# Kernel tuning notes

Hardware: AMD Instinct MI355X
Metric: run time of the kernel (lower is better)

Reference implementation:

```python
import jax, jax.numpy as jnp
import numpy as np

EPS = 1e-12  # matches F.normalize default eps

def _angle(e):
    # e: [N, D] embeddings
    d = e[:, None, :] - e[None, :, :]                      # [N, N, D] pairwise differences
    n = jnp.linalg.norm(d, axis=-1, keepdims=True)         # [N, N, 1]
    d = d / jnp.maximum(n, EPS)                            # normalized diffs; diagonal stays 0
    # all-triplet cosines: for each anchor i, Gram matrix of its normalized diffs
    return jnp.einsum('ijd,ikd->ijk', d, d)                # [N, N, N]

def _smooth_l1_mean(a, b):
    # torch F.smooth_l1_loss with beta=1.0, reduction='mean'
    x = jnp.abs(a - b)
    return jnp.mean(jnp.where(x < 1.0, 0.5 * x * x, x - 0.5))

def setup_inputs() -> dict:
    key = jax.random.key(0)
    k1, k2 = jax.random.split(key)
    student = jax.random.normal(k1, (384, 256), dtype=jnp.float32)
    teacher = jax.random.normal(k2, (384, 256), dtype=jnp.float32)
    return {"student": student, "teacher": teacher}

def reference(student, teacher):
    s_angle = _angle(student)
    t_angle = _angle(teacher)
    return _smooth_l1_mean(s_angle, t_angle)
```

## Files before the change

kernel.cpp:

```cpp
#include <hip/hip_runtime.h>
#include <hip/hip_bf16.h>

#define NPTS 384
#define NN (NPTS * NPTS)
#define DIMS 256
#define IT 8
#define NZI (NPTS / IT)

__global__ __launch_bounds__(1024) void gram_fused_kernel(
        const float* __restrict__ Es, const float* __restrict__ Et,
        float* __restrict__ Gs, float* __restrict__ Gt,
        float2* __restrict__ UHs, float2* __restrict__ UHt,
        float* __restrict__ out) {
    const int z = blockIdx.z;
    const float* __restrict__ E  = z ? Et : Es;
    float*       __restrict__ G  = z ? Gt : Gs;
    float2*      __restrict__ UH = z ? UHt : UHs;

    const int tx = threadIdx.x;
    const int ty = threadIdx.y;
    const int kc = threadIdx.z;
    const int t  = kc * 256 + ty * 16 + tx;
    const int i0 = blockIdx.x * 32;
    const int j0 = blockIdx.y * 32;

    if (blockIdx.x == 0 && blockIdx.y == 0 && z == 0 && t == 0) out[0] = 0.0f;

    __shared__ float sn[64];
    __shared__ float red[4][1024];

    {
        const int r = t >> 4;
        const int p = t & 15;
        const int row = (r < 32) ? (i0 + r) : (j0 + r - 32);
        const float4* __restrict__ src = (const float4*)(E + row * DIMS) + p * 4;
        float s = 0.f;
#pragma unroll
        for (int q = 0; q < 4; q++) {
            const float4 v = src[q];
            s += v.x * v.x + v.y * v.y + v.z * v.z + v.w * v.w;
        }
        s += __shfl_xor(s, 1, 64);
        s += __shfl_xor(s, 2, 64);
        s += __shfl_xor(s, 4, 64);
        s += __shfl_xor(s, 8, 64);
        if (p == 0) sn[r] = s;
    }

    const int i = i0 + 2 * ty;
    const int j = j0 + 2 * tx;
    const float4* __restrict__ a0 = (const float4*)(E + i * DIMS + kc * 64);
    const float4* __restrict__ a1 = (const float4*)(E + (i + 1) * DIMS + kc * 64);
    const float4* __restrict__ b0 = (const float4*)(E + j * DIMS + kc * 64);
    const float4* __restrict__ b1 = (const float4*)(E + (j + 1) * DIMS + kc * 64);

    float g00 = 0.f, g01 = 0.f, g10 = 0.f, g11 = 0.f;
#pragma unroll 4
    for (int k = 0; k < 16; k++) {
        const float4 av0 = a0[k], av1 = a1[k], bv0 = b0[k], bv1 = b1[k];
        g00 = fmaf(av0.x, bv0.x, g00); g00 = fmaf(av0.y, bv0.y, g00);
        g00 = fmaf(av0.z, bv0.z, g00); g00 = fmaf(av0.w, bv0.w, g00);
        g01 = fmaf(av0.x, bv1.x, g01); g01 = fmaf(av0.y, bv1.y, g01);
        g01 = fmaf(av0.z, bv1.z, g01); g01 = fmaf(av0.w, bv1.w, g01);
        g10 = fmaf(av1.x, bv0.x, g10); g10 = fmaf(av1.y, bv0.y, g10);
        g10 = fmaf(av1.z, bv0.z, g10); g10 = fmaf(av1.w, bv0.w, g10);
        g11 = fmaf(av1.x, bv1.x, g11); g11 = fmaf(av1.y, bv1.y, g11);
        g11 = fmaf(av1.z, bv1.z, g11); g11 = fmaf(av1.w, bv1.w, g11);
    }

    const int t2 = ty * 16 + tx;
    *(float4*)&red[kc][t2 * 4] = make_float4(g00, g01, g10, g11);
    __syncthreads();

    if (kc == 0) {
        const float4 r0 = *(const float4*)&red[0][t2 * 4];
        const float4 r1 = *(const float4*)&red[1][t2 * 4];
        const float4 r2 = *(const float4*)&red[2][t2 * 4];
        const float4 r3 = *(const float4*)&red[3][t2 * 4];
        const float g[2][2] = {{r0.x + r1.x + r2.x + r3.x, r0.y + r1.y + r2.y + r3.y},
                               {r0.z + r1.z + r2.z + r3.z, r0.w + r1.w + r2.w + r3.w}};
        const float si[2] = {sn[2 * ty], sn[2 * ty + 1]};
        const float sj[2] = {sn[32 + 2 * tx], sn[32 + 2 * tx + 1]};

#pragma unroll
        for (int r = 0; r < 2; r++) {
            const int ii = i + r;
            float uh[4];
#pragma unroll
            for (int c = 0; c < 2; c++) {
                const int jj = j + c;
                const float gv = g[r][c];
                const float v  = si[r] + sj[c] - 2.0f * gv;
                const float n  = sqrtf(fmaxf(v, 0.0f));
                uh[2 * c]     = (ii == jj) ? 0.0f : (1.0f / fmaxf(n, 1e-12f));
                uh[2 * c + 1] = 0.5f * si[r] - gv;
            }
            *(float2*)(G + ii * NPTS + j) = make_float2(g[r][0], g[r][1]);
            *(float4*)(UH + ii * NPTS + j) = make_float4(uh[0], uh[1], uh[2], uh[3]);
        }
    }
}

__global__ __launch_bounds__(256, 3) void rkd_main_kernel(
        const float* __restrict__ Gs, const float* __restrict__ Gt,
        const float2* __restrict__ UHs, const float2* __restrict__ UHt,
        float* __restrict__ out) {
    const int tlin = blockIdx.x;
    const int kt = (int)((sqrtf(8.0f * (float)tlin + 1.0f) - 1.0f) * 0.5f);
    const int jt = tlin - (kt * (kt + 1)) / 2;

    const int tx = threadIdx.x;
    const int ty = threadIdx.y;
    const int jb = jt * 64 + 4 * ty;
    const int kb = kt * 64 + 4 * tx;
    const int ibase = blockIdx.y * IT;

    float gs[4][4], gt[4][4];
#pragma unroll
    for (int a = 0; a < 4; a++) {
        const float4 vs = *(const float4*)(Gs + (jb + a) * NPTS + kb);
        const float4 vt = *(const float4*)(Gt + (jb + a) * NPTS + kb);
        gs[a][0] = vs.x; gs[a][1] = vs.y; gs[a][2] = vs.z; gs[a][3] = vs.w;
        gt[a][0] = vt.x; gt[a][1] = vt.y; gt[a][2] = vt.z; gt[a][3] = vt.w;
    }

    const float4* __restrict__ pjs = (const float4*)(UHs + (size_t)ibase * NPTS + jb);
    const float4* __restrict__ pjt = (const float4*)(UHt + (size_t)ibase * NPTS + jb);
    const float4* __restrict__ pks = (const float4*)(UHs + (size_t)ibase * NPTS + kb);
    const float4* __restrict__ pkt = (const float4*)(UHt + (size_t)ibase * NPTS + kb);

    const bool offd = (jt != kt);
    float wh[4][4];
#pragma unroll
    for (int a = 0; a < 4; a++)
#pragma unroll
        for (int b = 0; b < 4; b++) {
            const int jj = jb + a, kk = kb + b;
            wh[a][b] = (kk > jj) ? 1.0f : ((kk == jj) ? 0.5f : 0.0f);
        }

    float4 L[8];
    L[0] = pjs[0]; L[1] = pjs[1];
    L[2] = pjt[0]; L[3] = pjt[1];
    L[4] = pks[0]; L[5] = pks[1];
    L[6] = pkt[0]; L[7] = pkt[1];

    float acc = 0.0f;
#pragma unroll 2
    for (int iz = 0; iz < IT; iz++) {
        const int nz = (iz + 1 < IT) ? iz + 1 : iz;
        const int ro = nz * (NPTS / 2);
        float4 Ln[8];
        Ln[0] = pjs[ro];     Ln[1] = pjs[ro + 1];
        Ln[2] = pjt[ro];     Ln[3] = pjt[ro + 1];
        Ln[4] = pks[ro];     Ln[5] = pks[ro + 1];
        Ln[6] = pkt[ro];     Ln[7] = pkt[ro + 1];

        const float u_sj[4] = {L[0].x, L[0].z, L[1].x, L[1].z};
        const float h_sj[4] = {L[0].y, L[0].w, L[1].y, L[1].w};
        const float u_tj[4] = {L[2].x, L[2].z, L[3].x, L[3].z};
        const float h_tj[4] = {L[2].y, L[2].w, L[3].y, L[3].w};
        const float u_sk[4] = {L[4].x, L[4].z, L[5].x, L[5].z};
        const float h_sk[4] = {L[4].y, L[4].w, L[5].y, L[5].w};
        const float u_tk[4] = {L[6].x, L[6].z, L[7].x, L[7].z};
        const float h_tk[4] = {L[6].y, L[6].w, L[7].y, L[7].w};

        if (offd) {
#pragma unroll
            for (int a = 0; a < 4; a++) {
                const float usa = u_sj[a], hsa = h_sj[a];
                const float uta = u_tj[a], hta = h_tj[a];
#pragma unroll
                for (int b = 0; b < 4; b++) {
                    const float ts = gs[a][b] + hsa + h_sk[b];
                    const float tt = gt[a][b] + hta + h_tk[b];
                    const float ps = usa * u_sk[b];
                    const float pt = uta * u_tk[b];
                    const float mt = pt * tt;
                    const float d  = fmaf(ps, ts, -mt);
                    const float q  = d * d;
                    const float w  = fmaf(2.0f, fabsf(d), -1.0f);
                    acc += __builtin_amdgcn_fmed3f(q, w, 1.0f);
                }
            }
        } else {
#pragma unroll
            for (int a = 0; a < 4; a++) {
                const float usa = u_sj[a], hsa = h_sj[a];
                const float uta = u_tj[a], hta = h_tj[a];
#pragma unroll
                for (int b = 0; b < 4; b++) {
                    const float ts = gs[a][b] + hsa + h_sk[b];
                    const float tt = gt[a][b] + hta + h_tk[b];
                    const float ps = usa * u_sk[b];
                    const float pt = uta * u_tk[b];
                    const float mt = pt * tt;
                    const float d  = fmaf(ps, ts, -mt);
                    const float q  = d * d;
                    const float w  = fmaf(2.0f, fabsf(d), -1.0f);
                    const float l  = __builtin_amdgcn_fmed3f(q, w, 1.0f);
                    acc = fmaf(wh[a][b], l, acc);
                }
            }
        }

#pragma unroll
        for (int r = 0; r < 8; r++) L[r] = Ln[r];
    }

#pragma unroll
    for (int off = 32; off > 0; off >>= 1)
        acc += __shfl_down(acc, off, 64);

    __shared__ float wsum[4];
    const int tid  = ty * 16 + tx;
    const int wid  = tid >> 6;
    const int lane = tid & 63;
    if (lane == 0) wsum[wid] = acc;
    __syncthreads();
    if (tid == 0) {
        const float s = wsum[0] + wsum[1] + wsum[2] + wsum[3];
        atomicAdd(out, s * (1.0f / (384.0f * 384.0f * 384.0f)));
    }
}

extern "C" void kernel_launch(void* const* d_in, const int* in_sizes, int n_in,
                              void* d_out, int out_size, void* d_ws, size_t ws_size,
                              hipStream_t stream) {
    const float* student = (const float*)d_in[0];
    const float* teacher = (const float*)d_in[1];
    float* out = (float*)d_out;

    float*  Gs  = (float*)d_ws;
    float*  Gt  = Gs + NN;
    float2* UHs = (float2*)(Gt + NN);
    float2* UHt = UHs + NN;

    gram_fused_kernel<<<dim3(NPTS / 32, NPTS / 32, 2), dim3(16, 16, 4), 0, stream>>>(
        student, teacher, Gs, Gt, UHs, UHt, out);

    rkd_main_kernel<<<dim3(21, NZI), dim3(16, 16), 0, stream>>>(
        Gs, Gt, UHs, UHt, out);
}
```

Before: 114.5 us.

## Derive Gram tile from UH buffer and diagonal half-norms, halve i-tile, drop prefetch

The separate Gram matrices G are no longer written. The main kernel reconstructs the needed constant (0.5*|e_j|^2 - g) from the h field of UH plus a new per-point half-norm array. This removes two NN-sized global buffers and their writes. It also halves IT, which doubles the grid in the i dimension, removes the software prefetch double-buffer and the occupancy hint from launch bounds. The trade-off is more blocks, each reloading its j/k tiles, less latency hiding per thread, and reliance on the compiler for register allocation.

Result: slower. 138.3 us (+20.8%).

```diff
diff --git a/kernel.cpp b/kernel.cpp
--- a/kernel.cpp
+++ b/kernel.cpp
@@ -4,18 +4,18 @@
 #define NPTS 384
 #define NN (NPTS * NPTS)
 #define DIMS 256
-#define IT 8
+#define IT 4
 #define NZI (NPTS / IT)
 
 __global__ __launch_bounds__(1024) void gram_fused_kernel(
         const float* __restrict__ Es, const float* __restrict__ Et,
-        float* __restrict__ Gs, float* __restrict__ Gt,
         float2* __restrict__ UHs, float2* __restrict__ UHt,
+        float* __restrict__ HDs, float* __restrict__ HDt,
         float* __restrict__ out) {
     const int z = blockIdx.z;
     const float* __restrict__ E  = z ? Et : Es;
-    float*       __restrict__ G  = z ? Gt : Gs;
     float2*      __restrict__ UH = z ? UHt : UHs;
+    float*       __restrict__ HD = z ? HDt : HDs;
 
     const int tx = threadIdx.x;
     const int ty = threadIdx.y;
@@ -95,15 +95,15 @@
                 uh[2 * c]     = (ii == jj) ? 0.0f : (1.0f / fmaxf(n, 1e-12f));
                 uh[2 * c + 1] = 0.5f * si[r] - gv;
             }
-            *(float2*)(G + ii * NPTS + j) = make_float2(g[r][0], g[r][1]);
             *(float4*)(UH + ii * NPTS + j) = make_float4(uh[0], uh[1], uh[2], uh[3]);
         }
+        if (blockIdx.x == blockIdx.y && t2 < 32) HD[i0 + t2] = 0.5f * sn[t2];
     }
 }
 
-__global__ __launch_bounds__(256, 3) void rkd_main_kernel(
-        const float* __restrict__ Gs, const float* __restrict__ Gt,
+__global__ __launch_bounds__(256) void rkd_main_kernel(
         const float2* __restrict__ UHs, const float2* __restrict__ UHt,
+        const float* __restrict__ HDs, const float* __restrict__ HDt,
         float* __restrict__ out) {
     const int tlin = blockIdx.x;
     const int kt = (int)((sqrtf(8.0f * (float)tlin + 1.0f) - 1.0f) * 0.5f);
@@ -115,13 +115,18 @@
     const int kb = kt * 64 + 4 * tx;
     const int ibase = blockIdx.y * IT;
 
-    float gs[4][4], gt[4][4];
+    float cs[4][4], ct[4][4];
 #pragma unroll
     for (int a = 0; a < 4; a++) {
-        const float4 vs = *(const float4*)(Gs + (jb + a) * NPTS + kb);
-        const float4 vt = *(const float4*)(Gt + (jb + a) * NPTS + kb);
-        gs[a][0] = vs.x; gs[a][1] = vs.y; gs[a][2] = vs.z; gs[a][3] = vs.w;
-        gt[a][0] = vt.x; gt[a][1] = vt.y; gt[a][2] = vt.z; gt[a][3] = vt.w;
+        const float4* rs = (const float4*)(UHs + (jb + a) * NPTS + kb);
+        const float4* rt = (const float4*)(UHt + (jb + a) * NPTS + kb);
+        const float4 s0 = rs[0], s1 = rs[1];
+        const float4 t0 = rt[0], t1 = rt[1];
+        const float hds = HDs[jb + a], hdt = HDt[jb + a];
+        cs[a][0] = hds - s0.y; cs[a][1] = hds - s0.w;
+        cs[a][2] = hds - s1.y; cs[a][3] = hds - s1.w;
+        ct[a][0] = hdt - t0.y; ct[a][1] = hdt - t0.w;
+        ct[a][2] = hdt - t1.y; ct[a][3] = hdt - t1.w;
     }
 
     const float4* __restrict__ pjs = (const float4*)(UHs + (size_t)ibase * NPTS + jb);
@@ -139,31 +144,23 @@
             wh[a][b] = (kk > jj) ? 1.0f : ((kk == jj) ? 0.5f : 0.0f);
         }
 
-    float4 L[8];
-    L[0] = pjs[0]; L[1] = pjs[1];
-    L[2] = pjt[0]; L[3] = pjt[1];
-    L[4] = pks[0]; L[5] = pks[1];
-    L[6] = pkt[0]; L[7] = pkt[1];
-
     float acc = 0.0f;
 #pragma unroll 2
     for (int iz = 0; iz < IT; iz++) {
-        const int nz = (iz + 1 < IT) ? iz + 1 : iz;
-        const int ro = nz * (NPTS / 2);
-        float4 Ln[8];
-        Ln[0] = pjs[ro];     Ln[1] = pjs[ro + 1];
-        Ln[2] = pjt[ro];     Ln[3] = pjt[ro + 1];
-        Ln[4] = pks[ro];     Ln[5] = pks[ro + 1];
-        Ln[6] = pkt[ro];     Ln[7] = pkt[ro + 1];
-
-        const float u_sj[4] = {L[0].x, L[0].z, L[1].x, L[1].z};
-        const float h_sj[4] = {L[0].y, L[0].w, L[1].y, L[1].w};
-        const float u_tj[4] = {L[2].x, L[2].z, L[3].x, L[3].z};
-        const float h_tj[4] = {L[2].y, L[2].w, L[3].y, L[3].w};
-        const float u_sk[4] = {L[4].x, L[4].z, L[5].x, L[5].z};
-        const float h_sk[4] = {L[4].y, L[4].w, L[5].y, L[5].w};
-        const float u_tk[4] = {L[6].x, L[6].z, L[7].x, L[7].z};
-        const float h_tk[4] = {L[6].y, L[6].w, L[7].y, L[7].w};
+        const int ro = iz * (NPTS / 2);
+        const float4 js0 = pjs[ro], js1 = pjs[ro + 1];
+        const float4 jt0 = pjt[ro], jt1 = pjt[ro + 1];
+        const float4 ks0 = pks[ro], ks1 = pks[ro + 1];
+        const float4 kt0 = pkt[ro], kt1 = pkt[ro + 1];
+
+        const float u_sj[4] = {js0.x, js0.z, js1.x, js1.z};
+        const float h_sj[4] = {js0.y, js0.w, js1.y, js1.w};
+        const float u_tj[4] = {jt0.x, jt0.z, jt1.x, jt1.z};
+        const float h_tj[4] = {jt0.y, jt0.w, jt1.y, jt1.w};
+        const float u_sk[4] = {ks0.x, ks0.z, ks1.x, ks1.z};
+        const float h_sk[4] = {ks0.y, ks0.w, ks1.y, ks1.w};
+        const float u_tk[4] = {kt0.x, kt0.z, kt1.x, kt1.z};
+        const float h_tk[4] = {kt0.y, kt0.w, kt1.y, kt1.w};
 
         if (offd) {
 #pragma unroll
@@ -172,8 +169,8 @@
                 const float uta = u_tj[a], hta = h_tj[a];
 #pragma unroll
                 for (int b = 0; b < 4; b++) {
-                    const float ts = gs[a][b] + hsa + h_sk[b];
-                    const float tt = gt[a][b] + hta + h_tk[b];
+                    const float ts = cs[a][b] + hsa + h_sk[b];
+                    const float tt = ct[a][b] + hta + h_tk[b];
                     const float ps = usa * u_sk[b];
                     const float pt = uta * u_tk[b];
                     const float mt = pt * tt;
@@ -190,8 +187,8 @@
                 const float uta = u_tj[a], hta = h_tj[a];
 #pragma unroll
                 for (int b = 0; b < 4; b++) {
-                    const float ts = gs[a][b] + hsa + h_sk[b];
-                    const float tt = gt[a][b] + hta + h_tk[b];
+                    const float ts = cs[a][b] + hsa + h_sk[b];
+                    const float tt = ct[a][b] + hta + h_tk[b];
                     const float ps = usa * u_sk[b];
                     const float pt = uta * u_tk[b];
                     const float mt = pt * tt;
@@ -203,9 +200,6 @@
                 }
             }
         }
-
-#pragma unroll
-        for (int r = 0; r < 8; r++) L[r] = Ln[r];
     }
 
 #pragma unroll
@@ -231,14 +225,14 @@
     const float* teacher = (const float*)d_in[1];
     float* out = (float*)d_out;
 
-    float*  Gs  = (float*)d_ws;
-    float*  Gt  = Gs + NN;
-    float2* UHs = (float2*)(Gt + NN);
+    float2* UHs = (float2*)d_ws;
     float2* UHt = UHs + NN;
+    float*  HDs = (float*)(UHt + NN);
+    float*  HDt = HDs + NPTS;
 
     gram_fused_kernel<<<dim3(NPTS / 32, NPTS / 32, 2), dim3(16, 16, 4), 0, stream>>>(
-        student, teacher, Gs, Gt, UHs, UHt, out);
+        student, teacher, UHs, UHt, HDs, HDt, out);
 
     rkd_main_kernel<<<dim3(21, NZI), dim3(16, 16), 0, stream>>>(
-        Gs, Gt, UHs, UHt, out);
+        UHs, UHt, HDs, HDt, out);
 }
```
